# Kernel optimization log

Hardware: AMD Instinct MI355X
Metric: run time of the kernel (lower is better)

Reference implementation:

```python
import jax, jax.numpy as jnp
import numpy as np

N = 100000      # nodes
E = 3200000     # edges (avg degree 32)
IN = 256        # in_channels
OUT = 8         # out_channels
H1, C1 = 4, 4   # conv1: heads=4, out_channels=4 (concat -> 16)


def setup_inputs() -> dict:
    key = jax.random.key(0)
    ks = jax.random.split(key, 10)
    x = jax.random.normal(ks[0], (N, IN), jnp.float32)
    edge_index = jax.random.randint(ks[1], (2, E), 0, N, dtype=jnp.int64)

    def glorot(k, shape):
        fan_in = shape[0]
        return jax.random.normal(k, shape, jnp.float32) / np.float32(np.sqrt(fan_in))

    W1l = glorot(ks[2], (IN, H1 * C1))
    W1r = glorot(ks[3], (IN, H1 * C1))
    a1 = jax.random.normal(ks[4], (H1, C1), jnp.float32) / np.float32(np.sqrt(C1))
    b1 = jnp.zeros((H1 * C1,), jnp.float32)
    W2l = glorot(ks[5], (H1 * C1, OUT))
    W2r = glorot(ks[6], (H1 * C1, OUT))
    a2 = jax.random.normal(ks[7], (1, OUT), jnp.float32) / np.float32(np.sqrt(OUT))
    b2 = jnp.zeros((OUT,), jnp.float32)
    return {"x": x, "edge_index": edge_index, "W1l": W1l, "W1r": W1r, "a1": a1,
            "b1": b1, "W2l": W2l, "W2r": W2r, "a2": a2, "b2": b2}


def gatv2_conv(x, edge_index, Wl, Wr, att, bias, heads, ch, concat):
    # GATv2: e_ij = a^T LeakyReLU(Wl x_j + Wr x_i), softmax over incoming edges of i
    n = x.shape[0]
    src, dst = edge_index[0], edge_index[1]          # message flows src -> dst
    xl = (x @ Wl).reshape(n, heads, ch)              # [N,H,C] (source transform)
    xr = (x @ Wr).reshape(n, heads, ch)              # [N,H,C] (target transform)
    e = jax.nn.leaky_relu(xl[src] + xr[dst], 0.2)    # [E,H,C]
    logits = jnp.einsum('ehc,hc->eh', e, att)        # [E,H]
    # segment softmax over dst (stable: subtract per-target max)
    m = jax.ops.segment_max(logits, dst, num_segments=n)          # [N,H]
    ex = jnp.exp(logits - m[dst])                                  # [E,H]
    denom = jax.ops.segment_sum(ex, dst, num_segments=n)          # [N,H]
    alpha = ex / (denom[dst] + 1e-16)                              # [E,H]
    out = jax.ops.segment_sum(alpha[:, :, None] * xl[src], dst, num_segments=n)  # [N,H,C]
    out = out.reshape(n, heads * ch) if concat else out.mean(axis=1)
    return out + bias


def reference(x, edge_index, W1l, W1r, a1, b1, W2l, W2r, a2, b2):
    # eval mode: feature/attention dropout (p=0.6) are identity
    h = jax.nn.elu(gatv2_conv(x, edge_index, W1l, W1r, a1, b1, H1, C1, True))
    h = gatv2_conv(h, edge_index, W2l, W2r, a2, b2, 1, OUT, False)
    return jax.nn.sigmoid(h)
```

## Files before the change

### kernel.cpp

```cpp
#include <hip/hip_runtime.h>
#include <math.h>

#define NN 100000
#define NE 3200000
#define BW 512
#define BSH 9
#define NB 196
#define EPB_A 8192
#define NBLK_A ((NE + EPB_A - 1) / EPB_A)

__device__ __forceinline__ float lrelu(float v) { return v >= 0.f ? v : 0.2f * v; }


__global__ __launch_bounds__(256) void k_bhist(const int* __restrict__ dst,
                                               unsigned* __restrict__ btot) {
  __shared__ unsigned lh[NB];
  int tid = threadIdx.x;
  if (tid < NB) lh[tid] = 0;
  __syncthreads();
  int base = blockIdx.x * EPB_A;
  int end = min(base + EPB_A, NE);
  for (int e = base + tid * 4; e < end; e += 1024) {
    int4 d4 = *(const int4*)(dst + e);
    atomicAdd(&lh[((unsigned)d4.x) >> BSH], 1u);
    atomicAdd(&lh[((unsigned)d4.y) >> BSH], 1u);
    atomicAdd(&lh[((unsigned)d4.z) >> BSH], 1u);
    atomicAdd(&lh[((unsigned)d4.w) >> BSH], 1u);
  }
  __syncthreads();
  if (tid < NB && lh[tid]) atomicAdd(&btot[tid], lh[tid]);
}

__global__ __launch_bounds__(256) void k_bscan(const unsigned* __restrict__ btot,
    unsigned* __restrict__ bstart, unsigned* __restrict__ bcur) {
  __shared__ unsigned sm[256];
  int tid = threadIdx.x;
  unsigned v = (tid < NB) ? btot[tid] : 0;
  sm[tid] = v;
  __syncthreads();
  for (int off = 1; off < 256; off <<= 1) {
    unsigned u = (tid >= off) ? sm[tid - off] : 0;
    __syncthreads();
    sm[tid] += u;
    __syncthreads();
  }
  unsigned exc = sm[tid] - v;
  if (tid < NB) { bstart[tid] = exc; bcur[tid] = exc; }
  if (tid == NB - 1) bstart[NB] = sm[tid];
}

__global__ __launch_bounds__(256) void k_bin(const int* __restrict__ src,
    const int* __restrict__ dst, unsigned* __restrict__ bcur,
    unsigned* __restrict__ abuf) {
  __shared__ unsigned lh[NB], gb[NB], lcur[NB];
  int tid = threadIdx.x;
  if (tid < NB) lh[tid] = 0;
  __syncthreads();
  int base = blockIdx.x * EPB_A;
  int end = min(base + EPB_A, NE);
  for (int e = base + tid * 4; e < end; e += 1024) {
    int4 d4 = *(const int4*)(dst + e);
    atomicAdd(&lh[((unsigned)d4.x) >> BSH], 1u);
    atomicAdd(&lh[((unsigned)d4.y) >> BSH], 1u);
    atomicAdd(&lh[((unsigned)d4.z) >> BSH], 1u);
    atomicAdd(&lh[((unsigned)d4.w) >> BSH], 1u);
  }
  __syncthreads();
  if (tid < NB) {
    unsigned c = lh[tid];
    gb[tid] = c ? atomicAdd(&bcur[tid], c) : 0u;
    lcur[tid] = 0;
  }
  __syncthreads();
  for (int e = base + tid * 4; e < end; e += 1024) {
    int4 d4 = *(const int4*)(dst + e);
    int4 s4 = *(const int4*)(src + e);
    #pragma unroll
    for (int k = 0; k < 4; ++k) {
      unsigned d = (unsigned)(&d4.x)[k];
      unsigned s = (unsigned)(&s4.x)[k];
      unsigned b = d >> BSH;
      unsigned p = gb[b] + atomicAdd(&lcur[b], 1u);
      abuf[p] = ((d & (BW - 1)) << 17) | s;
    }
  }
}

__global__ __launch_bounds__(256) void k_bsort(const unsigned* __restrict__ bstart,
    const unsigned* __restrict__ abuf, int* __restrict__ rowstart,
    int* __restrict__ cnt, int* __restrict__ ssrc) {
  __shared__ unsigned lh[BW];
  __shared__ unsigned lcur[BW];
  __shared__ unsigned sm[256];
  int b = blockIdx.x, tid = threadIdx.x;
  unsigned s0 = bstart[b], s1 = bstart[b + 1];
  lh[tid] = 0; lh[tid + 256] = 0;
  __syncthreads();
  for (unsigned i = s0 + tid; i < s1; i += 256)
    atomicAdd(&lh[abuf[i] >> 17], 1u);
  __syncthreads();
  unsigned a0 = lh[2 * tid], a1 = lh[2 * tid + 1];
  sm[tid] = a0 + a1;
  __syncthreads();
  for (int off = 1; off < 256; off <<= 1) {
    unsigned u = (tid >= off) ? sm[tid - off] : 0;
    __syncthreads();
    sm[tid] += u;
    __syncthreads();
  }
  unsigned exc = sm[tid] - (a0 + a1);
  int node = b * BW + 2 * tid;
  if (node < NN)     { rowstart[node]     = s0 + exc;      cnt[node]     = a0; }
  if (node + 1 < NN) { rowstart[node + 1] = s0 + exc + a0; cnt[node + 1] = a1; }
  lcur[2 * tid] = exc;
  lcur[2 * tid + 1] = exc + a0;
  __syncthreads();
  for (unsigned i = s0 + tid; i < s1; i += 256) {
    unsigned v = abuf[i];
    unsigned p = s0 + atomicAdd(&lcur[v >> 17], 1u);
    ssrc[p] = (int)(v & 0x1FFFFu);
  }
}


__global__ __launch_bounds__(256) void k1_lin1(const float* __restrict__ x,
    const float* __restrict__ W1l, const float* __restrict__ W1r,
    float* __restrict__ xl1, float* __restrict__ xr1) {
  __shared__ float lw[256][32];
  int tid = threadIdx.x;
  for (int i = tid; i < 256 * 16; i += 256) {
    int k = i >> 4, c = i & 15;
    lw[k][c]      = W1l[i];
    lw[k][16 + c] = W1r[i];
  }
  __syncthreads();
  int row = blockIdx.x * 256 + tid;
  if (row >= NN) return;
  const float4* xr4 = (const float4*)(x + (size_t)row * 256);

  float acc[32];
  #pragma unroll
  for (int c = 0; c < 32; ++c) acc[c] = 0.f;

  float4 va = xr4[0], vb = xr4[1];
  for (int k4 = 0; k4 < 64; k4 += 2) {
    float4 vc = xr4[(k4 + 2) & 63];
    float4 vd = xr4[(k4 + 3) & 63];
    #pragma unroll
    for (int half = 0; half < 2; ++half) {
      float4 v = half ? vb : va;
      int kb = (k4 + half) * 4;
      #pragma unroll
      for (int kk = 0; kk < 4; ++kk) {
        float xk = (&v.x)[kk];
        const float4* wrow = (const float4*)&lw[kb + kk][0];
        #pragma unroll
        for (int q = 0; q < 8; ++q) {
          float4 w = wrow[q];
          acc[q * 4 + 0] = fmaf(xk, w.x, acc[q * 4 + 0]);
          acc[q * 4 + 1] = fmaf(xk, w.y, acc[q * 4 + 1]);
          acc[q * 4 + 2] = fmaf(xk, w.z, acc[q * 4 + 2]);
          acc[q * 4 + 3] = fmaf(xk, w.w, acc[q * 4 + 3]);
        }
      }
    }
    va = vc; vb = vd;
  }
  float4* ol = (float4*)(xl1 + (size_t)row * 16);
  float4* orr = (float4*)(xr1 + (size_t)row * 16);
  #pragma unroll
  for (int q = 0; q < 4; ++q) {
    ol[q]  = make_float4(acc[q*4+0], acc[q*4+1], acc[q*4+2], acc[q*4+3]);
    orr[q] = make_float4(acc[16+q*4+0], acc[16+q*4+1], acc[16+q*4+2], acc[16+q*4+3]);
  }
}


__global__ __launch_bounds__(256) void k_l1(const float* __restrict__ xl1,
    const float* __restrict__ xr1, const float* __restrict__ a1,
    const float* __restrict__ b1, const float* __restrict__ W2l,
    const float* __restrict__ W2r, const int* __restrict__ rowstart,
    const int* __restrict__ cnt, const int* __restrict__ ssrc,
    float* __restrict__ xl2, float* __restrict__ xr2) {
  __shared__ float w2[16][16];
  int tid = threadIdx.x;
  if (tid < 128) {
    int k = tid >> 3, c = tid & 7;
    w2[k][c]     = W2l[tid];
    w2[k][8 + c] = W2r[tid];
  }
  __syncthreads();
  int i = (blockIdx.x * 256 + tid) >> 6;
  if (i >= NN) return;
  int lane = tid & 63;
  int j = lane >> 2, h = lane & 3;

  float4 xr = *(const float4*)(xr1 + (size_t)i * 16 + h * 4);
  float4 av = *(const float4*)(a1 + h * 4);
  int rs = rowstart[i], deg = cnt[i];

  float m = -INFINITY, den = 0.f;
  float4 acc = make_float4(0.f, 0.f, 0.f, 0.f);

  for (int base = 0; base < deg; base += 16) {
    int jj = base + j;
    bool valid = jj < deg;
    int s = valid ? ssrc[rs + jj] : 0;
    float4 xl = make_float4(0.f, 0.f, 0.f, 0.f);
    if (valid) xl = *(const float4*)(xl1 + (size_t)s * 16 + h * 4);
    float lg = valid ? (lrelu(xl.x + xr.x) * av.x + lrelu(xl.y + xr.y) * av.y +
                        lrelu(xl.z + xr.z) * av.z + lrelu(xl.w + xr.w) * av.w)
                     : -INFINITY;
    float mp = lg;
    mp = fmaxf(mp, __shfl_xor(mp, 4));
    mp = fmaxf(mp, __shfl_xor(mp, 8));
    mp = fmaxf(mp, __shfl_xor(mp, 16));
    mp = fmaxf(mp, __shfl_xor(mp, 32));
    float nm = fmaxf(m, mp);
    float r = __expf(m - nm);
    float p = __expf(lg - nm);
    m = nm;
    den = den * r + p;
    acc.x = acc.x * r + p * xl.x;
    acc.y = acc.y * r + p * xl.y;
    acc.z = acc.z * r + p * xl.z;
    acc.w = acc.w * r + p * xl.w;
  }
  #pragma unroll
  for (int st = 4; st <= 32; st <<= 1) {
    den   += __shfl_xor(den, st);
    acc.x += __shfl_xor(acc.x, st);
    acc.y += __shfl_xor(acc.y, st);
    acc.z += __shfl_xor(acc.z, st);
    acc.w += __shfl_xor(acc.w, st);
  }
  float4 bv = *(const float4*)(b1 + h * 4);
  float inv = 1.f / (den + 1e-16f);
  float q0 = acc.x * inv + bv.x;
  float q1 = acc.y * inv + bv.y;
  float q2 = acc.z * inv + bv.z;
  float q3 = acc.w * inv + bv.w;
  q0 = q0 > 0.f ? q0 : expm1f(q0);
  q1 = q1 > 0.f ? q1 : expm1f(q1);
  q2 = q2 > 0.f ? q2 : expm1f(q2);
  q3 = q3 > 0.f ? q3 : expm1f(q3);

  float hh[16];
  #pragma unroll
  for (int hp = 0; hp < 4; ++hp) {
    hh[hp * 4 + 0] = __shfl(q0, hp);
    hh[hp * 4 + 1] = __shfl(q1, hp);
    hh[hp * 4 + 2] = __shfl(q2, hp);
    hh[hp * 4 + 3] = __shfl(q3, hp);
  }
  int t = lane & 15;
  float val = 0.f;
  #pragma unroll
  for (int k = 0; k < 16; ++k) val = fmaf(hh[k], w2[k][t], val);
  if (lane < 8)       xl2[(size_t)i * 8 + lane] = val;
  else if (lane < 16) xr2[(size_t)i * 8 + (lane - 8)] = val;
}


__global__ __launch_bounds__(256) void k_l2(const float* __restrict__ xl2,
    const float* __restrict__ xr2, const float* __restrict__ a2,
    const float* __restrict__ b2, const int* __restrict__ rowstart,
    const int* __restrict__ cnt, const int* __restrict__ ssrc,
    float* __restrict__ out) {
  int tid = threadIdx.x;
  int i = (blockIdx.x * 256 + tid) >> 6;
  if (i >= NN) return;
  int lane = tid & 63;

  float xr[8], av[8];
  *(float4*)&xr[0] = *(const float4*)(xr2 + (size_t)i * 8);
  *(float4*)&xr[4] = *(const float4*)(xr2 + (size_t)i * 8 + 4);
  *(float4*)&av[0] = *(const float4*)(a2);
  *(float4*)&av[4] = *(const float4*)(a2 + 4);
  int rs = rowstart[i], deg = cnt[i];

  float m = -INFINITY, den = 0.f, acc[8];
  #pragma unroll
  for (int c = 0; c < 8; ++c) acc[c] = 0.f;

  for (int base = 0; base < deg; base += 64) {
    int jj = base + lane;
    bool valid = jj < deg;
    int s = valid ? ssrc[rs + jj] : 0;
    float xl[8];
    #pragma unroll
    for (int c = 0; c < 8; ++c) xl[c] = 0.f;
    if (valid) {
      *(float4*)&xl[0] = *(const float4*)(xl2 + (size_t)s * 8);
      *(float4*)&xl[4] = *(const float4*)(xl2 + (size_t)s * 8 + 4);
    }
    float lg;
    if (valid) {
      lg = 0.f;
      #pragma unroll
      for (int c = 0; c < 8; ++c) lg += lrelu(xl[c] + xr[c]) * av[c];
    } else lg = -INFINITY;
    float mp = lg;
    #pragma unroll
    for (int st = 1; st <= 32; st <<= 1) mp = fmaxf(mp, __shfl_xor(mp, st));
    float nm = fmaxf(m, mp);
    float r = __expf(m - nm);
    float p = __expf(lg - nm);
    m = nm;
    den = den * r + p;
    #pragma unroll
    for (int c = 0; c < 8; ++c) acc[c] = acc[c] * r + p * xl[c];
  }
  #pragma unroll
  for (int st = 1; st <= 32; st <<= 1) {
    den += __shfl_xor(den, st);
    #pragma unroll
    for (int c = 0; c < 8; ++c) acc[c] += __shfl_xor(acc[c], st);
  }
  if (lane == 0) {
    float inv = 1.f / (den + 1e-16f);
    float o[8];
    #pragma unroll
    for (int c = 0; c < 8; ++c) {
      float v = acc[c] * inv + b2[c];
      o[c] = 1.f / (1.f + __expf(-v));
    }
    *(float4*)(out + (size_t)i * 8)     = make_float4(o[0], o[1], o[2], o[3]);
    *(float4*)(out + (size_t)i * 8 + 4) = make_float4(o[4], o[5], o[6], o[7]);
  }
}


extern "C" void kernel_launch(void* const* d_in, const int* in_sizes, int n_in,
                              void* d_out, int out_size, void* d_ws, size_t ws_size,
                              hipStream_t stream) {
  const float* x   = (const float*)d_in[0];
  const int*   ei  = (const int*)d_in[1];
  const float* W1l = (const float*)d_in[2];
  const float* W1r = (const float*)d_in[3];
  const float* a1  = (const float*)d_in[4];
  const float* b1  = (const float*)d_in[5];
  const float* W2l = (const float*)d_in[6];
  const float* W2r = (const float*)d_in[7];
  const float* a2  = (const float*)d_in[8];
  const float* b2  = (const float*)d_in[9];
  const int* src = ei;
  const int* dst = ei + NE;

  char* ws = (char*)d_ws;
  size_t off = 0;
  auto alloc = [&](size_t bytes) { void* p = (void*)(ws + off); off += (bytes + 255) & ~(size_t)255; return p; };
  unsigned* btot   = (unsigned*)alloc((size_t)NB * 4);
  unsigned* bstart = (unsigned*)alloc((size_t)(NB + 1) * 4);
  unsigned* bcur   = (unsigned*)alloc((size_t)NB * 4);
  int*      rowstart = (int*)alloc((size_t)NN * 4);
  int*      cnt      = (int*)alloc((size_t)NN * 4);
  int*      ssrc     = (int*)alloc((size_t)NE * 4);
  char*     bigbase  = (char*)alloc((size_t)NN * 16 * 4 * 2);
  unsigned* abuf = (unsigned*)bigbase;
  float*    xl1  = (float*)bigbase;
  float*    xr1  = (float*)(bigbase + (size_t)NN * 16 * 4);
  float*    xl2  = (float*)alloc((size_t)NN * 8 * 4);
  float*    xr2  = (float*)alloc((size_t)NN * 8 * 4);

  hipMemsetAsync(btot, 0, (size_t)NB * 4, stream);

  k_bhist<<<NBLK_A, 256, 0, stream>>>(dst, btot);
  k_bscan<<<1, 256, 0, stream>>>(btot, bstart, bcur);
  k_bin  <<<NBLK_A, 256, 0, stream>>>(src, dst, bcur, abuf);
  k_bsort<<<NB, 256, 0, stream>>>(bstart, abuf, rowstart, cnt, ssrc);

  k1_lin1<<<(NN + 255) / 256, 256, 0, stream>>>(x, W1l, W1r, xl1, xr1);

  int gw = (NN * 64 + 255) / 256;
  k_l1<<<gw, 256, 0, stream>>>(xl1, xr1, a1, b1, W2l, W2r, rowstart, cnt, ssrc, xl2, xr2);
  k_l2<<<gw, 256, 0, stream>>>(xl2, xr2, a2, b2, rowstart, cnt, ssrc, (float*)d_out);
}
```

Baseline: 433.5 us.

## Drop max-subtraction in softmax, split layer-2 linear into own kernel, remap k_l2 lanes

The online max-tracking softmax in both attention kernels is replaced by a plain exp-sum with no max subtraction. This removes the shuffle max-reductions and rescale multiplies, but exp can overflow if logits grow large. The layer-2 linear transform moves out of k_l1 into a new per-node kernel k5_mid, which adds an intermediate buffer round-trip through memory. k_l2 is remapped from one edge per lane to 8 edges by 8 channels per wavefront, so each lane issues a single scalar gather.

```diff
diff --git a/kernel.cpp b/kernel.cpp
--- a/kernel.cpp
+++ b/kernel.cpp
@@ -178,18 +178,10 @@
 
 __global__ __launch_bounds__(256) void k_l1(const float* __restrict__ xl1,
     const float* __restrict__ xr1, const float* __restrict__ a1,
-    const float* __restrict__ b1, const float* __restrict__ W2l,
-    const float* __restrict__ W2r, const int* __restrict__ rowstart,
+    const float* __restrict__ b1, const int* __restrict__ rowstart,
     const int* __restrict__ cnt, const int* __restrict__ ssrc,
-    float* __restrict__ xl2, float* __restrict__ xr2) {
-  __shared__ float w2[16][16];
-  int tid = threadIdx.x;
-  if (tid < 128) {
-    int k = tid >> 3, c = tid & 7;
-    w2[k][c]     = W2l[tid];
-    w2[k][8 + c] = W2r[tid];
-  }
-  __syncthreads();
+    float* __restrict__ hbuf) {
+  int tid = threadIdx.x;
   int i = (blockIdx.x * 256 + tid) >> 6;
   if (i >= NN) return;
   int lane = tid & 63;
@@ -199,32 +191,22 @@
   float4 av = *(const float4*)(a1 + h * 4);
   int rs = rowstart[i], deg = cnt[i];
 
-  float m = -INFINITY, den = 0.f;
+  float den = 0.f;
   float4 acc = make_float4(0.f, 0.f, 0.f, 0.f);
 
   for (int base = 0; base < deg; base += 16) {
     int jj = base + j;
     bool valid = jj < deg;
     int s = valid ? ssrc[rs + jj] : 0;
-    float4 xl = make_float4(0.f, 0.f, 0.f, 0.f);
-    if (valid) xl = *(const float4*)(xl1 + (size_t)s * 16 + h * 4);
-    float lg = valid ? (lrelu(xl.x + xr.x) * av.x + lrelu(xl.y + xr.y) * av.y +
-                        lrelu(xl.z + xr.z) * av.z + lrelu(xl.w + xr.w) * av.w)
-                     : -INFINITY;
-    float mp = lg;
-    mp = fmaxf(mp, __shfl_xor(mp, 4));
-    mp = fmaxf(mp, __shfl_xor(mp, 8));
-    mp = fmaxf(mp, __shfl_xor(mp, 16));
-    mp = fmaxf(mp, __shfl_xor(mp, 32));
-    float nm = fmaxf(m, mp);
-    float r = __expf(m - nm);
-    float p = __expf(lg - nm);
-    m = nm;
-    den = den * r + p;
-    acc.x = acc.x * r + p * xl.x;
-    acc.y = acc.y * r + p * xl.y;
-    acc.z = acc.z * r + p * xl.z;
-    acc.w = acc.w * r + p * xl.w;
+    float4 xl = *(const float4*)(xl1 + (size_t)s * 16 + h * 4);
+    float lg = lrelu(xl.x + xr.x) * av.x + lrelu(xl.y + xr.y) * av.y +
+               lrelu(xl.z + xr.z) * av.z + lrelu(xl.w + xr.w) * av.w;
+    float p = valid ? __expf(lg) : 0.f;
+    den += p;
+    acc.x = fmaf(p, xl.x, acc.x);
+    acc.y = fmaf(p, xl.y, acc.y);
+    acc.z = fmaf(p, xl.z, acc.z);
+    acc.w = fmaf(p, xl.w, acc.w);
   }
   #pragma unroll
   for (int st = 4; st <= 32; st <<= 1) {
@@ -234,31 +216,55 @@
     acc.z += __shfl_xor(acc.z, st);
     acc.w += __shfl_xor(acc.w, st);
   }
-  float4 bv = *(const float4*)(b1 + h * 4);
-  float inv = 1.f / (den + 1e-16f);
-  float q0 = acc.x * inv + bv.x;
-  float q1 = acc.y * inv + bv.y;
-  float q2 = acc.z * inv + bv.z;
-  float q3 = acc.w * inv + bv.w;
-  q0 = q0 > 0.f ? q0 : expm1f(q0);
-  q1 = q1 > 0.f ? q1 : expm1f(q1);
-  q2 = q2 > 0.f ? q2 : expm1f(q2);
-  q3 = q3 > 0.f ? q3 : expm1f(q3);
-
+  if (j == 0) {
+    float inv = 1.f / (den + 1e-16f);
+    float4 bv = *(const float4*)(b1 + h * 4);
+    float v0 = fmaf(acc.x, inv, bv.x);
+    float v1 = fmaf(acc.y, inv, bv.y);
+    float v2 = fmaf(acc.z, inv, bv.z);
+    float v3 = fmaf(acc.w, inv, bv.w);
+    v0 = v0 > 0.f ? v0 : __expf(v0) - 1.f;
+    v1 = v1 > 0.f ? v1 : __expf(v1) - 1.f;
+    v2 = v2 > 0.f ? v2 : __expf(v2) - 1.f;
+    v3 = v3 > 0.f ? v3 : __expf(v3) - 1.f;
+    *(float4*)(hbuf + (size_t)i * 16 + h * 4) = make_float4(v0, v1, v2, v3);
+  }
+}
+
+
+__global__ __launch_bounds__(256) void k5_mid(const float* __restrict__ hbuf,
+    const float* __restrict__ W2l, const float* __restrict__ W2r,
+    float* __restrict__ xl2, float* __restrict__ xr2) {
+  __shared__ float w2[16][16];
+  int tid = threadIdx.x;
+  if (tid < 128) {
+    int k = tid >> 3, c = tid & 7;
+    w2[k][c]     = W2l[tid];
+    w2[k][8 + c] = W2r[tid];
+  }
+  __syncthreads();
+  int n = blockIdx.x * 256 + tid;
+  if (n >= NN) return;
   float hh[16];
-  #pragma unroll
-  for (int hp = 0; hp < 4; ++hp) {
-    hh[hp * 4 + 0] = __shfl(q0, hp);
-    hh[hp * 4 + 1] = __shfl(q1, hp);
-    hh[hp * 4 + 2] = __shfl(q2, hp);
-    hh[hp * 4 + 3] = __shfl(q3, hp);
-  }
-  int t = lane & 15;
-  float val = 0.f;
-  #pragma unroll
-  for (int k = 0; k < 16; ++k) val = fmaf(hh[k], w2[k][t], val);
-  if (lane < 8)       xl2[(size_t)i * 8 + lane] = val;
-  else if (lane < 16) xr2[(size_t)i * 8 + (lane - 8)] = val;
+  const float4* hp = (const float4*)(hbuf + (size_t)n * 16);
+  #pragma unroll
+  for (int q = 0; q < 4; ++q) *(float4*)&hh[q * 4] = hp[q];
+  float ol[8], orr[8];
+  #pragma unroll
+  for (int jq = 0; jq < 8; ++jq) { ol[jq] = 0.f; orr[jq] = 0.f; }
+  #pragma unroll
+  for (int k = 0; k < 16; ++k) {
+    float hv = hh[k];
+    #pragma unroll
+    for (int jq = 0; jq < 8; ++jq) {
+      ol[jq]  = fmaf(hv, w2[k][jq], ol[jq]);
+      orr[jq] = fmaf(hv, w2[k][8 + jq], orr[jq]);
+    }
+  }
+  *(float4*)(xl2 + (size_t)n * 8)     = make_float4(ol[0], ol[1], ol[2], ol[3]);
+  *(float4*)(xl2 + (size_t)n * 8 + 4) = make_float4(ol[4], ol[5], ol[6], ol[7]);
+  *(float4*)(xr2 + (size_t)n * 8)     = make_float4(orr[0], orr[1], orr[2], orr[3]);
+  *(float4*)(xr2 + (size_t)n * 8 + 4) = make_float4(orr[4], orr[5], orr[6], orr[7]);
 }
 
 
@@ -271,62 +277,34 @@
   int i = (blockIdx.x * 256 + tid) >> 6;
   if (i >= NN) return;
   int lane = tid & 63;
-
-  float xr[8], av[8];
-  *(float4*)&xr[0] = *(const float4*)(xr2 + (size_t)i * 8);
-  *(float4*)&xr[4] = *(const float4*)(xr2 + (size_t)i * 8 + 4);
-  *(float4*)&av[0] = *(const float4*)(a2);
-  *(float4*)&av[4] = *(const float4*)(a2 + 4);
+  int j = lane >> 3, c = lane & 7;
+
+  float xrc = xr2[(size_t)i * 8 + c];
+  float avc = a2[c];
   int rs = rowstart[i], deg = cnt[i];
 
-  float m = -INFINITY, den = 0.f, acc[8];
-  #pragma unroll
-  for (int c = 0; c < 8; ++c) acc[c] = 0.f;
-
-  for (int base = 0; base < deg; base += 64) {
-    int jj = base + lane;
+  float den = 0.f, accc = 0.f;
+  for (int base = 0; base < deg; base += 8) {
+    int jj = base + j;
     bool valid = jj < deg;
     int s = valid ? ssrc[rs + jj] : 0;
-    float xl[8];
-    #pragma unroll
-    for (int c = 0; c < 8; ++c) xl[c] = 0.f;
-    if (valid) {
-      *(float4*)&xl[0] = *(const float4*)(xl2 + (size_t)s * 8);
-      *(float4*)&xl[4] = *(const float4*)(xl2 + (size_t)s * 8 + 4);
-    }
-    float lg;
-    if (valid) {
-      lg = 0.f;
-      #pragma unroll
-      for (int c = 0; c < 8; ++c) lg += lrelu(xl[c] + xr[c]) * av[c];
-    } else lg = -INFINITY;
-    float mp = lg;
-    #pragma unroll
-    for (int st = 1; st <= 32; st <<= 1) mp = fmaxf(mp, __shfl_xor(mp, st));
-    float nm = fmaxf(m, mp);
-    float r = __expf(m - nm);
-    float p = __expf(lg - nm);
-    m = nm;
-    den = den * r + p;
-    #pragma unroll
-    for (int c = 0; c < 8; ++c) acc[c] = acc[c] * r + p * xl[c];
-  }
-  #pragma unroll
-  for (int st = 1; st <= 32; st <<= 1) {
-    den += __shfl_xor(den, st);
-    #pragma unroll
-    for (int c = 0; c < 8; ++c) acc[c] += __shfl_xor(acc[c], st);
-  }
-  if (lane == 0) {
-    float inv = 1.f / (den + 1e-16f);
-    float o[8];
-    #pragma unroll
-    for (int c = 0; c < 8; ++c) {
-      float v = acc[c] * inv + b2[c];
-      o[c] = 1.f / (1.f + __expf(-v));
-    }
-    *(float4*)(out + (size_t)i * 8)     = make_float4(o[0], o[1], o[2], o[3]);
-    *(float4*)(out + (size_t)i * 8 + 4) = make_float4(o[4], o[5], o[6], o[7]);
+    float xlc = xl2[(size_t)s * 8 + c];
+    float lg = lrelu(xlc + xrc) * avc;
+    lg += __shfl_xor(lg, 1);
+    lg += __shfl_xor(lg, 2);
+    lg += __shfl_xor(lg, 4);
+    float p = valid ? __expf(lg) : 0.f;
+    den += p;
+    accc = fmaf(p, xlc, accc);
+  }
+  #pragma unroll
+  for (int st = 8; st <= 32; st <<= 1) {
+    den  += __shfl_xor(den, st);
+    accc += __shfl_xor(accc, st);
+  }
+  if (j == 0) {
+    float v = accc / (den + 1e-16f) + b2[c];
+    out[(size_t)i * 8 + c] = 1.f / (1.f + __expf(-v));
   }
 }
 
@@ -362,6 +340,7 @@
   float*    xr1  = (float*)(bigbase + (size_t)NN * 16 * 4);
   float*    xl2  = (float*)alloc((size_t)NN * 8 * 4);
   float*    xr2  = (float*)alloc((size_t)NN * 8 * 4);
+  float*    hbuf = (float*)alloc((size_t)NN * 16 * 4);
 
   hipMemsetAsync(btot, 0, (size_t)NB * 4, stream);
 
@@ -373,6 +352,7 @@
   k1_lin1<<<(NN + 255) / 256, 256, 0, stream>>>(x, W1l, W1r, xl1, xr1);
 
   int gw = (NN * 64 + 255) / 256;
-  k_l1<<<gw, 256, 0, stream>>>(xl1, xr1, a1, b1, W2l, W2r, rowstart, cnt, ssrc, xl2, xr2);
+  k_l1<<<gw, 256, 0, stream>>>(xl1, xr1, a1, b1, rowstart, cnt, ssrc, hbuf);
+  k5_mid<<<(NN + 255) / 256, 256, 0, stream>>>(hbuf, W2l, W2r, xl2, xr2);
   k_l2<<<gw, 256, 0, stream>>>(xl2, xr2, a2, b2, rowstart, cnt, ssrc, (float*)d_out);
 }
```

Result: faster. 412.8 us (-4.8%).
